# Kernel optimization log

Measured on AMD Instinct MI355X. Metric: run time of the kernel, lower is better.

The kernel has to match this reference:

```python
import jax, jax.numpy as jnp
import numpy as np

V, D, Z, C = 50000, 300, 128, 10

def setup_inputs() -> dict:
    key = jax.random.key(0)
    ks = jax.random.split(key, 12)
    idxs = jax.random.randint(ks[0], (C,), 0, V)
    center_idx = jax.random.randint(ks[1], (), 0, V)
    center_word = jnp.zeros((V,), jnp.float32).at[center_idx].set(1.0)  # one-hot [V]
    context_words = jnp.zeros((C, V), jnp.float32).at[jnp.arange(C), idxs].set(1.0)  # one-hot [C,V]
    s = 0.05
    return {
        "center_word": center_word,
        "context_words": context_words,
        "context_word_idxs": idxs,
        "eps": jax.random.normal(ks[2], (Z,), jnp.float32),
        "E": jax.random.normal(ks[3], (D, V), jnp.float32) * s,
        "W_mu": jax.random.normal(ks[4], (Z, 2 * D), jnp.float32) * s,
        "b_mu": jnp.zeros((Z,), jnp.float32),
        "W_sig": jax.random.normal(ks[5], (Z, 2 * D), jnp.float32) * s,
        "b_sig": jnp.zeros((Z,), jnp.float32),
        "prior_mean": jax.random.normal(ks[6], (Z, V), jnp.float32) * s,
        "prior_sigma": jax.random.normal(ks[7], (Z, V), jnp.float32) * s,
        "W_gen": jax.random.normal(ks[8], (V, Z), jnp.float32) * s,
        "b_gen": jnp.zeros((V,), jnp.float32),
    }


def reference(center_word, context_words, context_word_idxs, eps,
              E, W_mu, b_mu, W_sig, b_sig, prior_mean, prior_sigma, W_gen, b_gen):
    # One-hot matmul 'lookups' (faithful to original dense matmuls)
    ce = center_word @ E.T                      # [D]
    cw = context_words @ E.T                    # [C, D]
    cat = jnp.concatenate([jnp.broadcast_to(ce, (cw.shape[0], ce.shape[0])), cw], axis=1)  # [C, 2D]
    summed = jax.nn.relu(cat).sum(0)            # [2D]
    u = W_mu @ summed + b_mu                    # [Z]
    s = jax.nn.softplus(W_sig @ summed + b_sig)  # [Z]
    z = u + eps * s                             # reparameterized sample [Z]
    logprobs = jax.nn.log_softmax(W_gen @ z + b_gen)  # [V]
    # prior (note: original computes z_mean but never uses it in the KL)
    z_sigma = jax.nn.softplus(center_word @ prior_sigma.T)  # [Z]
    loss_probs = logprobs[context_word_idxs]    # gather [C]
    kl = jnp.log(z_sigma / s) + (s**2 + (u - z_sigma) ** 2) / (2.0 * z_sigma**2) - 0.5
    return loss_probs.sum() - kl.sum()
```

## Files before the change

kernel.cpp:

```cpp
#include <hip/hip_runtime.h>
#include <float.h>
#include <math.h>

#define V 50000
#define D 300
#define Z 128
#define C 10
#define TWOD 600
#define NENC 32
#define RWE 8
#define RPB 64
#define NCON 782
#define FINAL_BID (NENC + NCON)
#define NBLK (FINAL_BID + 1)
#define NREP 16
#define MAGIC 0x5F3C7A91u

typedef unsigned long long u64;


__device__ __forceinline__ float softplusf(float x) {
    return log1pf(expf(-fabsf(x))) + fmaxf(x, 0.0f);
}
__device__ __forceinline__ void st_u32(unsigned* p, unsigned v) {
    __hip_atomic_store(p, v, __ATOMIC_RELAXED, __HIP_MEMORY_SCOPE_AGENT);
}
__device__ __forceinline__ unsigned ld_u32(const unsigned* p) {
    return __hip_atomic_load(p, __ATOMIC_RELAXED, __HIP_MEMORY_SCOPE_AGENT);
}
__device__ __forceinline__ void st_tag(u64* p, float x) {
    u64 v = ((u64)MAGIC << 32) | (u64)__float_as_uint(x);
    __hip_atomic_store(p, v, __ATOMIC_RELAXED, __HIP_MEMORY_SCOPE_AGENT);
}
__device__ __forceinline__ float poll_tag(u64* p) {
    u64 v;
    for (;;) {
        v = __hip_atomic_load(p, __ATOMIC_RELAXED, __HIP_MEMORY_SCOPE_AGENT);
        if ((unsigned)(v >> 32) == MAGIC) break;
        __builtin_amdgcn_s_sleep(1);
    }
    return __uint_as_float((unsigned)v);
}
__device__ __forceinline__ void gload16(const void* g, void* l) {
    __builtin_amdgcn_global_load_lds(
        (const __attribute__((address_space(1))) void*)g,
        (__attribute__((address_space(3))) void*)l,
        16, 0, 0);
}

__global__ __launch_bounds__(256, 4) void k_all(
        const float* __restrict__ cw,
        const float* __restrict__ E,
        const int* __restrict__ idxs,
        const float* __restrict__ Wmu, const float* __restrict__ bmu,
        const float* __restrict__ Wsig, const float* __restrict__ bsig,
        const float* __restrict__ eps,
        const float* __restrict__ psig,
        const float* __restrict__ Wgen, const float* __restrict__ bgen,
        char* __restrict__ ws, float* __restrict__ out) {
    unsigned* cidx_enc = (unsigned*)(ws + 0);
    u64*      rawtag   = (u64*)(ws + 4096);
    u64*      bmbs     = (u64*)(ws + 270336);
    u64*      gslots   = (u64*)(ws + 286720);
    u64*      klslot   = (u64*)(ws + 290816);

    __shared__ __align__(16) float wtile[RPB * Z];
    __shared__ float summed[TWOD];
    __shared__ float rawv[2 * Z];
    __shared__ __align__(16) float zsh[Z];
    __shared__ float lsh[RPB];
    __shared__ float bgsh[RPB];
    __shared__ int sidx[C];
    __shared__ float red_m[4], red_s[4], klred[2];
    __shared__ int scidx;

    int bid = blockIdx.x, tid = threadIdx.x;
    int w = tid >> 6, l = tid & 63;
    if (tid < C) sidx[tid] = idxs[tid];

    if (bid < NENC) {
        if (tid == 0) {
            unsigned e;
            for (;;) {
                e = ld_u32(cidx_enc);
                if (e - MAGIC < (unsigned)V) break;
                __builtin_amdgcn_s_sleep(1);
            }
            scidx = (int)(e - MAGIC);
        }
        __syncthreads();
        int cidx = scidx;
        for (int d = tid; d < D; d += 256) {
            float ce = E[(size_t)d * V + cidx];
            summed[d] = (float)C * fmaxf(ce, 0.0f);
            float acc = 0.0f;
            #pragma unroll
            for (int c = 0; c < C; ++c)
                acc += fmaxf(E[(size_t)d * V + sidx[c]], 0.0f);
            summed[D + d] = acc;
        }
        __syncthreads();
        float val0, val1;
        #pragma unroll
        for (int rr = 0; rr < 2; ++rr) {
            int r = bid * RWE + w * 2 + rr;
            const float* Wrow; float bias;
            if (r < Z) { Wrow = Wmu  + (size_t)r * TWOD;       bias = bmu[r]; }
            else       { Wrow = Wsig + (size_t)(r - Z) * TWOD; bias = bsig[r - Z]; }
            float acc = 0.0f;
            for (int k = l; k < TWOD; k += 64) acc += Wrow[k] * summed[k];
            #pragma unroll
            for (int off = 32; off; off >>= 1) acc += __shfl_xor(acc, off);
            if (rr == 0) val0 = acc + bias; else val1 = acc + bias;
        }
        if (l < 32) {
            int rr  = l >> 4, rep = l & 15;
            int r   = bid * RWE + w * 2 + rr;
            float v = (l < 16) ? val0 : val1;
            st_tag(rawtag + (size_t)(rep * 256 + r) * 8, v);
        }
        return;
    }

    if (bid == FINAL_BID) {
        float fm = -FLT_MAX, fs = 0.0f;
        for (int t = tid; t < NCON; t += 256) {
            float m2 = poll_tag(bmbs + 2 * (size_t)t);
            float s2 = poll_tag(bmbs + 2 * (size_t)t + 1);
            float M = fmaxf(fm, m2);
            fs = fs * expf(fm - M) + s2 * expf(m2 - M);
            fm = M;
        }
        #pragma unroll
        for (int off = 32; off; off >>= 1) {
            float m2 = __shfl_xor(fm, off), s2 = __shfl_xor(fs, off);
            float M = fmaxf(fm, m2);
            fs = fs * expf(fm - M) + s2 * expf(m2 - M);
            fm = M;
        }
        if (l == 0) { red_m[w] = fm; red_s[w] = fs; }
        __syncthreads();
        if (tid == 0) {
            float M = red_m[0], S = red_s[0];
            #pragma unroll
            for (int w2 = 1; w2 < 4; ++w2) {
                float m2 = red_m[w2], s2 = red_s[w2];
                float Mn = fmaxf(M, m2);
                S = S * expf(M - Mn) + s2 * expf(m2 - Mn);
                M = Mn;
            }
            float lse = M + logf(S);
            float g = 0.0f;
            #pragma unroll
            for (int c = 0; c < C; ++c) g += poll_tag(gslots + (size_t)c * 8);
            float kls = poll_tag(klslot);
            out[0] = g - (float)C * lse - kls;
        }
        return;
    }

    int c = bid - NENC;
    int g = c * 256 + tid;
    if (g < V / 4) {
        float4 wv = ((const float4*)cw)[g];
        int found = -1;
        if      (wv.x != 0.0f) found = 4 * g + 0;
        else if (wv.y != 0.0f) found = 4 * g + 1;
        else if (wv.z != 0.0f) found = 4 * g + 2;
        else if (wv.w != 0.0f) found = 4 * g + 3;
        if (found >= 0) st_u32(cidx_enc, (unsigned)found + MAGIC);
    }

    int base = c * RPB;
    {
        const char* gw = (const char*)Wgen + ((size_t)base + (size_t)w * 16) * 512;
        #pragma unroll
        for (int i = 0; i < 8; ++i) {
            int row0 = base + w * 16 + 2 * i;
            const char* src = (row0 + 2 <= V) ? gw + i * 1024
                                              : (const char*)Wgen;
            gload16(src + l * 16, &wtile[w * 2048 + i * 256]);
        }
    }
    if (tid < RPB) {
        int rr = base + tid;
        bgsh[tid] = bgen[rr < V ? rr : V - 1];
    }
    float ev = (tid < Z) ? eps[tid] : 0.0f;

    rawv[tid] = poll_tag(rawtag + (size_t)((bid & (NREP - 1)) * 256 + tid) * 8);
    if (c == 0 && tid == 0) {
        unsigned e;
        for (;;) {
            e = ld_u32(cidx_enc);
            if (e - MAGIC < (unsigned)V) break;
            __builtin_amdgcn_s_sleep(1);
        }
        scidx = (int)(e - MAGIC);
    }
    __syncthreads();

    if (tid < Z) {
        float u = rawv[tid];
        float s = softplusf(rawv[Z + tid]);
        zsh[tid] = u + ev * s;
        if (c == 0) {
            float zs = softplusf(psig[(size_t)tid * V + scidx]);
            float kl = logf(zs / s) + (s * s + (u - zs) * (u - zs)) / (2.0f * zs * zs) - 0.5f;
            #pragma unroll
            for (int off = 32; off; off >>= 1) kl += __shfl_xor(kl, off);
            if (l == 0) klred[w] = kl;
        }
    }
    __syncthreads();
    if (c == 0 && tid == 0) st_tag(klslot, klred[0] + klred[1]);

    asm volatile("s_waitcnt vmcnt(0)" ::: "memory");
    float4 zreg = ((const float4*)zsh)[l & 31];
    #pragma unroll
    for (int i = 0; i < 8; ++i) {
        const float4 wv = *(const float4*)&wtile[w * 2048 + i * 256
                                                 + (l >> 5) * 128 + (l & 31) * 4];
        float p = wv.x * zreg.x + wv.y * zreg.y + wv.z * zreg.z + wv.w * zreg.w;
        p += __shfl_xor(p, 1);  p += __shfl_xor(p, 2);  p += __shfl_xor(p, 4);
        p += __shfl_xor(p, 8);  p += __shfl_xor(p, 16);
        if ((l & 31) == 0) {
            int rloc = w * 16 + 2 * i + (l >> 5);
            int row = base + rloc;
            lsh[rloc] = (row < V) ? (p + bgsh[rloc]) : -FLT_MAX;
        }
    }
    __syncthreads();

    if (w == 0) {
        float lg = lsh[l];
        float m = lg, s = (lg > -FLT_MAX) ? 1.0f : 0.0f;
        #pragma unroll
        for (int off = 32; off; off >>= 1) {
            float m2 = __shfl_xor(m, off), s2 = __shfl_xor(s, off);
            float M = fmaxf(m, m2);
            s = s * expf(m - M) + s2 * expf(m2 - M);
            m = M;
        }
        if (l == 0) {
            st_tag(bmbs + 2 * (size_t)c, m);
            st_tag(bmbs + 2 * (size_t)c + 1, s);
        }
    }
    if (tid < RPB) {
        int row = base + tid;
        if (row < V) {
            float lg = lsh[tid];
            #pragma unroll
            for (int cc = 0; cc < C; ++cc)
                if (row == sidx[cc]) st_tag(gslots + (size_t)cc * 8, lg);
        }
    }
}

extern "C" void kernel_launch(void* const* d_in, const int* in_sizes, int n_in,
                              void* d_out, int out_size, void* d_ws, size_t ws_size,
                              hipStream_t stream) {
    const float* center = (const float*)d_in[0];
    const int*   idxs   = (const int*)d_in[2];
    const float* eps    = (const float*)d_in[3];
    const float* E      = (const float*)d_in[4];
    const float* Wmu    = (const float*)d_in[5];
    const float* bmu    = (const float*)d_in[6];
    const float* Wsig   = (const float*)d_in[7];
    const float* bsig   = (const float*)d_in[8];
    const float* psig   = (const float*)d_in[10];
    const float* Wgen   = (const float*)d_in[11];
    const float* bgen   = (const float*)d_in[12];

    k_all<<<NBLK, 256, 0, stream>>>(center, E, idxs, Wmu, bmu, Wsig, bsig,
                                    eps, psig, Wgen, bgen,
                                    (char*)d_ws, (float*)d_out);
}
```

Before: 16.88 us.

## Precompute context half of encoder before waiting on center index; batch final-block tag loads

Encoder blocks now prefetch their weight rows into registers and compute the context-word relu sums and their half of the dot products before spinning on the center-index flag. Only the center-word half is done after the index arrives, which takes work off the dependency chain. The final block issues all its partial-result tag loads up front and only falls back to polling for slots not yet ready, instead of polling each slot in sequence. This costs extra register pressure and an additional __syncthreads.

```diff
diff --git a/kernel.cpp b/kernel.cpp
--- a/kernel.cpp
+++ b/kernel.cpp
@@ -28,6 +28,9 @@
 __device__ __forceinline__ unsigned ld_u32(const unsigned* p) {
     return __hip_atomic_load(p, __ATOMIC_RELAXED, __HIP_MEMORY_SCOPE_AGENT);
 }
+__device__ __forceinline__ u64 ld_u64(const u64* p) {
+    return __hip_atomic_load(p, __ATOMIC_RELAXED, __HIP_MEMORY_SCOPE_AGENT);
+}
 __device__ __forceinline__ void st_tag(u64* p, float x) {
     u64 v = ((u64)MAGIC << 32) | (u64)__float_as_uint(x);
     __hip_atomic_store(p, v, __ATOMIC_RELAXED, __HIP_MEMORY_SCOPE_AGENT);
@@ -40,6 +43,10 @@
         __builtin_amdgcn_s_sleep(1);
     }
     return __uint_as_float((unsigned)v);
+}
+__device__ __forceinline__ float finish_tag(u64 v, u64* p) {
+    return ((unsigned)(v >> 32) == MAGIC) ? __uint_as_float((unsigned)v)
+                                          : poll_tag(p);
 }
 __device__ __forceinline__ void gload16(const void* g, void* l) {
     __builtin_amdgcn_global_load_lds(
@@ -79,6 +86,35 @@
     if (tid < C) sidx[tid] = idxs[tid];
 
     if (bid < NENC) {
+        int r0 = bid * RWE + w * 2, r1 = r0 + 1;
+        const float* W0; const float* W1; float b0, b1;
+        if (r0 < Z) { W0 = Wmu + (size_t)r0 * TWOD;        b0 = bmu[r0]; }
+        else        { W0 = Wsig + (size_t)(r0 - Z) * TWOD; b0 = bsig[r0 - Z]; }
+        if (r1 < Z) { W1 = Wmu + (size_t)r1 * TWOD;        b1 = bmu[r1]; }
+        else        { W1 = Wsig + (size_t)(r1 - Z) * TWOD; b1 = bsig[r1 - Z]; }
+
+        float w0c[5], w1c[5];
+        #pragma unroll
+        for (int i = 0; i < 5; ++i) {
+            int k = l + i * 64;
+            w0c[i] = (k < D) ? W0[k] : 0.0f;
+            w1c[i] = (k < D) ? W1[k] : 0.0f;
+        }
+        __syncthreads();
+        for (int d = tid; d < D; d += 256) {
+            float acc = 0.0f;
+            #pragma unroll
+            for (int c = 0; c < C; ++c)
+                acc += fmaxf(E[(size_t)d * V + sidx[c]], 0.0f);
+            summed[D + d] = acc;
+        }
+        __syncthreads();
+        float p0 = 0.0f, p1 = 0.0f;
+        for (int k = l; k < D; k += 64) {
+            float s = summed[D + k];
+            p0 += W0[D + k] * s;
+            p1 += W1[D + k] * s;
+        }
         if (tid == 0) {
             unsigned e;
             for (;;) {
@@ -90,32 +126,27 @@
         }
         __syncthreads();
         int cidx = scidx;
-        for (int d = tid; d < D; d += 256) {
-            float ce = E[(size_t)d * V + cidx];
-            summed[d] = (float)C * fmaxf(ce, 0.0f);
-            float acc = 0.0f;
-            #pragma unroll
-            for (int c = 0; c < C; ++c)
-                acc += fmaxf(E[(size_t)d * V + sidx[c]], 0.0f);
-            summed[D + d] = acc;
-        }
-        __syncthreads();
-        float val0, val1;
-        #pragma unroll
-        for (int rr = 0; rr < 2; ++rr) {
-            int r = bid * RWE + w * 2 + rr;
-            const float* Wrow; float bias;
-            if (r < Z) { Wrow = Wmu  + (size_t)r * TWOD;       bias = bmu[r]; }
-            else       { Wrow = Wsig + (size_t)(r - Z) * TWOD; bias = bsig[r - Z]; }
-            float acc = 0.0f;
-            for (int k = l; k < TWOD; k += 64) acc += Wrow[k] * summed[k];
-            #pragma unroll
-            for (int off = 32; off; off >>= 1) acc += __shfl_xor(acc, off);
-            if (rr == 0) val0 = acc + bias; else val1 = acc + bias;
-        }
+        for (int d = tid; d < D; d += 256)
+            summed[d] = (float)C * fmaxf(E[(size_t)d * V + cidx], 0.0f);
+        __syncthreads();
+        #pragma unroll
+        for (int i = 0; i < 5; ++i) {
+            int k = l + i * 64;
+            if (k < D) {
+                float s = summed[k];
+                p0 += w0c[i] * s;
+                p1 += w1c[i] * s;
+            }
+        }
+        #pragma unroll
+        for (int off = 32; off; off >>= 1) {
+            p0 += __shfl_xor(p0, off);
+            p1 += __shfl_xor(p1, off);
+        }
+        float val0 = p0 + b0, val1 = p1 + b1;
         if (l < 32) {
-            int rr  = l >> 4, rep = l & 15;
-            int r   = bid * RWE + w * 2 + rr;
+            int rep = l & 15;
+            int r   = (l < 16) ? r0 : r1;
             float v = (l < 16) ? val0 : val1;
             st_tag(rawtag + (size_t)(rep * 256 + r) * 8, v);
         }
@@ -123,13 +154,26 @@
     }
 
     if (bid == FINAL_BID) {
+        u64 vm[4], vs[4];
+        #pragma unroll
+        for (int i = 0; i < 4; ++i) {
+            int t = tid + i * 256;
+            if (t < NCON) {
+                vm[i] = ld_u64(bmbs + 2 * (size_t)t);
+                vs[i] = ld_u64(bmbs + 2 * (size_t)t + 1);
+            }
+        }
         float fm = -FLT_MAX, fs = 0.0f;
-        for (int t = tid; t < NCON; t += 256) {
-            float m2 = poll_tag(bmbs + 2 * (size_t)t);
-            float s2 = poll_tag(bmbs + 2 * (size_t)t + 1);
-            float M = fmaxf(fm, m2);
-            fs = fs * expf(fm - M) + s2 * expf(m2 - M);
-            fm = M;
+        #pragma unroll
+        for (int i = 0; i < 4; ++i) {
+            int t = tid + i * 256;
+            if (t < NCON) {
+                float m2 = finish_tag(vm[i], bmbs + 2 * (size_t)t);
+                float s2 = finish_tag(vs[i], bmbs + 2 * (size_t)t + 1);
+                float M = fmaxf(fm, m2);
+                fs = fs * expf(fm - M) + s2 * expf(m2 - M);
+                fm = M;
+            }
         }
         #pragma unroll
         for (int off = 32; off; off >>= 1) {
```

New measurement: 14.22 us. 15.7% less time.
